# Kernel optimization log

Hardware: AMD Instinct MI355X
Metric: run time of the kernel (lower is better)

The kernel has to match this reference:

```python
import jax, jax.numpy as jnp
import numpy as np

B, N, K, CLS = 256, 15, 520, 800  # batch, points per streamline, k+k_global, classes
EPS = 1e-5


def _bn(x, g, b, m, v, axis=1):
    # eval-mode BatchNorm with running stats
    shape = [1] * x.ndim
    shape[axis] = -1
    rs = lambda a: a.reshape(shape)
    return rs(g) * (x - rs(m)) * jax.lax.rsqrt(rs(v) + EPS) + rs(b)


def setup_inputs():
    key = jax.random.key(0)
    kit = iter(jax.random.split(key, 24))
    nk = lambda: next(kit)
    p = {}
    p["pts"] = jax.random.normal(nk(), (B, N, 3), jnp.float32)
    p["label"] = jax.random.randint(nk(), (B,), 0, CLS)
    p["info_point_set"] = jax.random.normal(nk(), (B, K, N, 3), jnp.float32)

    def lin(cout, cin):
        w = jax.random.normal(nk(), (cout, cin), jnp.float32) * (1.0 / np.sqrt(cin))
        return w, jnp.zeros((cout,), jnp.float32)

    def bn(c):
        return (jnp.ones((c,), jnp.float32), jnp.zeros((c,), jnp.float32),
                jax.random.normal(nk(), (c,), jnp.float32) * 0.05,
                jnp.ones((c,), jnp.float32))

    p["w_info"], p["b_info"] = lin(64, 6)
    p["g_info"], p["be_info"], p["m_info"], p["v_info"] = bn(64)
    p["w2"], p["b2"] = lin(128, 64)
    p["g2"], p["be2"], p["m2"], p["v2"] = bn(128)
    p["w3"], p["b3"] = lin(1024, 128)
    p["g3"], p["be3"], p["m3"], p["v3"] = bn(1024)
    p["wf1"], p["bf1"] = lin(512, 1024)
    p["gf1"], p["bef1"], p["mf1"], p["vf1"] = bn(512)
    p["wf2"], p["bf2"] = lin(256, 512)
    p["gf2"], p["bef2"], p["mf2"], p["vf2"] = bn(256)
    p["wf3"], p["bf3"] = lin(CLS, 256)
    return p


def reference(pts, label, info_point_set,
              w_info, b_info, g_info, be_info, m_info, v_info,
              w2, b2, g2, be2, m2, v2,
              w3, b3, g3, be3, m3, v3,
              wf1, bf1, gf1, bef1, mf1, vf1,
              wf2, bf2, gf2, bef2, mf2, vf2,
              wf3, bf3):
    x = jnp.transpose(pts, (0, 2, 1))                      # [B,3,N]
    ips = jnp.transpose(info_point_set, (0, 3, 2, 1))      # [B,3,N,K]
    xr = jnp.broadcast_to(x[..., None], ips.shape)         # [B,3,N,K]
    h = jnp.concatenate([ips - xr, xr], axis=1)            # [B,6,N,K]
    h = jnp.einsum('oc,bcnk->bonk', w_info, h) + b_info[None, :, None, None]
    h = jax.nn.relu(_bn(h, g_info, be_info, m_info, v_info))
    h = jnp.max(h, axis=-1)                                # [B,64,N]  (max over neighbors)
    h2 = jax.nn.relu(_bn(jnp.einsum('oc,bcn->bon', w2, h) + b2[None, :, None],
                         g2, be2, m2, v2))                 # [B,128,N]
    h3 = _bn(jnp.einsum('oc,bcn->bon', w3, h2) + b3[None, :, None],
             g3, be3, m3, v3)                              # [B,1024,N]
    g = jnp.max(h3, axis=2)                                # [B,1024] global max-pool
    f1 = jax.nn.relu(_bn(g @ wf1.T + bf1, gf1, bef1, mf1, vf1, axis=1))
    f2 = jax.nn.relu(_bn(f1 @ wf2.T + bf2, gf2, bef2, mf2, vf2, axis=1))  # dropout identity (eval)
    ret = f2 @ wf3.T + bf3                                 # [B,CLS]
    return (ret, f2)
```

## Files before the change

### kernel.cpp

```cpp
#include <hip/hip_runtime.h>
#include <math.h>

#define EPS 1e-5f

typedef __attribute__((ext_vector_type(8))) short short8v;
typedef __attribute__((ext_vector_type(4))) float f32x4;
typedef __attribute__((ext_vector_type(16))) float f32x16;

__device__ __forceinline__ unsigned short bf16r(float x) {
    unsigned u = __float_as_uint(x);
    return (unsigned short)((u + 0x7FFFu + ((u >> 16) & 1u)) >> 16);
}
__device__ __forceinline__ float bf2f(unsigned short h) {
    return __uint_as_float(((unsigned)h) << 16);
}
__device__ __forceinline__ unsigned packhl(float x) {
    const unsigned short h = bf16r(x);
    const unsigned short l = bf16r(x - bf2f(h));
    return (unsigned)h | ((unsigned)l << 16);
}

__global__ __launch_bounds__(256) void k_pre(
    const float* __restrict__ w3, const float* __restrict__ b3,
    const float* __restrict__ g3, const float* __restrict__ be3,
    const float* __restrict__ m3, const float* __restrict__ v3,
    const float* __restrict__ w2, const float* __restrict__ b2,
    const float* __restrict__ g2, const float* __restrict__ be2,
    const float* __restrict__ m2, const float* __restrict__ v2,
    const float* __restrict__ w_info, const float* __restrict__ b_info,
    const float* __restrict__ g_info, const float* __restrict__ be_info,
    const float* __restrict__ m_info, const float* __restrict__ v_info,
    const float* __restrict__ bf1, const float* __restrict__ gf1,
    const float* __restrict__ bef1, const float* __restrict__ mf1,
    const float* __restrict__ vf1,
    const float* __restrict__ bf2, const float* __restrict__ gf2,
    const float* __restrict__ bef2, const float* __restrict__ mf2,
    const float* __restrict__ vf2,
    const float* __restrict__ wf1, const float* __restrict__ wf2,
    const float* __restrict__ wf3,
    unsigned short* __restrict__ Bh, unsigned short* __restrict__ Bl,
    float* __restrict__ bias3,
    float4* __restrict__ w2q, float* __restrict__ bias2,
    unsigned short* __restrict__ Bedge,
    float4* __restrict__ qTab4,
    float* __restrict__ sf1, float* __restrict__ cf1,
    float* __restrict__ sf2, float* __restrict__ cf2,
    unsigned short* __restrict__ B1h, unsigned short* __restrict__ B1l,
    unsigned short* __restrict__ B2h, unsigned short* __restrict__ B2l,
    unsigned short* __restrict__ B3h, unsigned short* __restrict__ B3l)
{
    const int blk = blockIdx.x, tid = threadIdx.x;
    if (blk < 64) {
        const int t = blk * 256 + tid;
        const int kt = t >> 12;
        const int nt = (t >> 6) & 63;
        const int lane = t & 63;
        const int o  = nt * 16 + (lane & 15);
        const int kb = kt * 32 + ((lane >> 4) << 3);
        const float a3 = g3[o] * rsqrtf(v3[o] + EPS);
        #pragma unroll
        for (int j = 0; j < 8; ++j) {
            const float wv = a3 * w3[(size_t)o * 128 + kb + j];
            const unsigned short hi = bf16r(wv);
            Bh[(size_t)t * 8 + j] = hi;
            Bl[(size_t)t * 8 + j] = bf16r(wv - bf2f(hi));
        }
    } else if (blk == 64) {
        for (int idx = tid; idx < 2048; idx += 256) {
            const int o2 = idx & 127, cq = idx >> 7;
            const float a2 = g2[o2] * rsqrtf(v2[o2] + EPS);
            const float4 w = *(const float4*)(w2 + (size_t)o2 * 64 + cq * 4);
            w2q[cq * 128 + o2] = make_float4(a2 * w.x, a2 * w.y, a2 * w.z, a2 * w.w);
        }
        if (tid < 128) {
            const float a2 = g2[tid] * rsqrtf(v2[tid] + EPS);
            bias2[tid] = a2 * (b2[tid] - m2[tid]) + be2[tid];
        }
    } else if (blk == 65) {
        if (tid < 128) {
            const int nt = tid >> 6, lane = tid & 63;
            const int grp = lane >> 5;
            const int o = nt * 32 + (lane & 31);
            const float a = g_info[o] * rsqrtf(v_info[o] + EPS);
            const float c0 = a * w_info[o*6+0];
            const float c1 = a * w_info[o*6+1];
            const float c2 = a * w_info[o*6+2];
            const unsigned short ch0 = bf16r(c0), ch1 = bf16r(c1), ch2 = bf16r(c2);
            const unsigned short cl0 = bf16r(c0 - bf2f(ch0));
            const unsigned short cl1 = bf16r(c1 - bf2f(ch1));
            const unsigned short cl2 = bf16r(c2 - bf2f(ch2));
            unsigned short out[8] = {0,0,0,0,0,0,0,0};
            if (grp == 0) {
                out[0]=ch0; out[1]=ch1; out[2]=ch2;
                out[3]=cl0; out[4]=cl1; out[5]=cl2;
                out[6]=ch0; out[7]=ch1;
            } else {
                out[0]=ch2;
            }
            #pragma unroll
            for (int j = 0; j < 8; ++j)
                Bedge[(size_t)(nt*64 + lane)*8 + j] = out[j];
        }
        if (tid < 64) {
            const int o = tid;
            const float w0 = w_info[o*6+0], w1 = w_info[o*6+1], w2c = w_info[o*6+2];
            const float w3c = w_info[o*6+3], w4 = w_info[o*6+4], w5 = w_info[o*6+5];
            const float a = g_info[o] * rsqrtf(v_info[o] + EPS);
            qTab4[o] = make_float4(a*(w3c-w0), a*(w4-w1), a*(w5-w2c),
                                   a*(b_info[o]-m_info[o]) + be_info[o]);
        }
        for (int c = tid; c < 1024; c += 256) {
            const float a3 = g3[c] * rsqrtf(v3[c] + EPS);
            bias3[c] = a3 * (b3[c] - m3[c]) + be3[c];
        }
        for (int c = tid; c < 512; c += 256) {
            const float s = gf1[c] * rsqrtf(vf1[c] + EPS);
            sf1[c] = s;
            cf1[c] = s * (bf1[c] - mf1[c]) + bef1[c];
        }
        {
            const int c = tid;
            const float s = gf2[c] * rsqrtf(vf2[c] + EPS);
            sf2[c] = s;
            cf2[c] = s * (bf2[c] - mf2[c]) + bef2[c];
        }
    } else if (blk < 322) {
        const int idx = (blk - 66) * 256 + tid;
        const int lane = idx & 63;
        const int nt = (idx >> 6) & 15;
        const int kt = idx >> 10;
        const int n  = nt * 32 + (lane & 31);
        const int kb = kt * 16 + ((lane >> 5) << 3);
        #pragma unroll
        for (int j = 0; j < 8; ++j) {
            const float wv = wf1[(size_t)n * 1024 + kb + j];
            const unsigned short hi = bf16r(wv);
            B1h[(size_t)idx * 8 + j] = hi;
            B1l[(size_t)idx * 8 + j] = bf16r(wv - bf2f(hi));
        }
    } else if (blk < 386) {
        const int idx = (blk - 322) * 256 + tid;
        const int lane = idx & 63;
        const int nt = (idx >> 6) & 7;
        const int kt = idx >> 9;
        const int n  = nt * 32 + (lane & 31);
        const int kb = kt * 16 + ((lane >> 5) << 3);
        #pragma unroll
        for (int j = 0; j < 8; ++j) {
            const float wv = wf2[(size_t)n * 512 + kb + j];
            const unsigned short hi = bf16r(wv);
            B2h[(size_t)idx * 8 + j] = hi;
            B2l[(size_t)idx * 8 + j] = bf16r(wv - bf2f(hi));
        }
    } else {
        const int idx = (blk - 386) * 256 + tid;
        const int lane = idx & 63;
        const int g6 = idx >> 6;
        const int nt = g6 % 25;
        const int kt = g6 / 25;
        const int n  = nt * 32 + (lane & 31);
        const int kb = kt * 16 + ((lane >> 5) << 3);
        #pragma unroll
        for (int j = 0; j < 8; ++j) {
            const float wv = wf3[(size_t)n * 256 + kb + j];
            const unsigned short hi = bf16r(wv);
            B3h[(size_t)idx * 8 + j] = hi;
            B3l[(size_t)idx * 8 + j] = bf16r(wv - bf2f(hi));
        }
    }
}

__global__ __launch_bounds__(960) void k_edgeS3(
    const float* __restrict__ pts,
    const float* __restrict__ info,
    const unsigned short* __restrict__ Bedge,
    const float4* __restrict__ qTab4,
    const float4* __restrict__ w2q,
    const float* __restrict__ bias2,
    const unsigned short* __restrict__ Bh,
    const unsigned short* __restrict__ Bl,
    const float* __restrict__ bias3,
    unsigned short* __restrict__ ghi,
    unsigned short* __restrict__ glo)
{
    __shared__ unsigned dsb[23400];
    __shared__ float h1s[960];
    __shared__ unsigned short h2hL[2048];
    __shared__ unsigned short h2lL[2048];

    const int tid = threadIdx.x;
    const int b = blockIdx.x;

    {
        const float4* src = (const float4*)(info + (size_t)b * 23400);
        uint4* dst = (uint4*)dsb;
        for (int i = tid; i < 5850; i += 960) {
            const float4 v = src[i];
            uint4 pv;
            pv.x = packhl(v.x); pv.y = packhl(v.y);
            pv.z = packhl(v.z); pv.w = packhl(v.w);
            dst[i] = pv;
        }
    }
    __syncthreads();

    const int wave = tid >> 6, lane = tid & 63;
    const int la = lane & 31;
    const bool hiHalf = lane >= 32;

    {
        short8v bfrag0 = *(const short8v*)(Bedge + (size_t)(0*64 + lane)*8);
        short8v bfrag1 = *(const short8v*)(Bedge + (size_t)(1*64 + lane)*8);

        const f32x16 zero16 = {0.f,0.f,0.f,0.f,0.f,0.f,0.f,0.f,
                               0.f,0.f,0.f,0.f,0.f,0.f,0.f,0.f};

        {
            const int n = wave;
            float m0 = -INFINITY, m1 = -INFINITY;
            const unsigned* pb = dsb + n*3;

            unsigned w0 = 0, w1 = 0, w2 = 0;
            {
                const unsigned* p = pb + la*45;
                if (!hiHalf) { w0 = p[0]; w1 = p[1]; }
                w2 = p[2];
            }

            #pragma unroll 1
            for (int mt = 0; mt < 17; ++mt) {
                unsigned nw0 = 0, nw1 = 0, nw2 = 0;
                if (mt < 16) {
                    int nrow = (mt+1)*32 + la;
                    nrow = nrow > 519 ? 519 : nrow;
                    const unsigned* p = pb + nrow*45;
                    if (!hiHalf) { nw0 = p[0]; nw1 = p[1]; }
                    nw2 = p[2];
                }
                int4 ai;
                if (!hiHalf) {
                    ai.x = (int)((w0 & 0xFFFFu) | (w1 << 16));
                    ai.y = (int)((w2 & 0xFFFFu) | (w0 << 16));
                    ai.z = (int)((w1 & 0xFFFFu) | (w2 << 16));
                    ai.w = (int)((w0 >> 16) | (w1 & 0xFFFF0000u));
                } else {
                    ai.x = (int)(w2 >> 16);
                    ai.y = 0; ai.z = 0; ai.w = 0;
                }
                const short8v afrag = *(short8v*)&ai;
                const f32x16 r0 = __builtin_amdgcn_mfma_f32_32x32x16_bf16(afrag, bfrag0, zero16, 0,0,0);
                const f32x16 r1 = __builtin_amdgcn_mfma_f32_32x32x16_bf16(afrag, bfrag1, zero16, 0,0,0);
                #pragma unroll
                for (int c = 0; c < 16; c += 4) {
                    m0 = fmaxf(m0, fmaxf(fmaxf(r0[c], r0[c+1]),
                                         fmaxf(r0[c+2], r0[c+3])));
                    m1 = fmaxf(m1, fmaxf(fmaxf(r1[c], r1[c+1]),
                                         fmaxf(r1[c+2], r1[c+3])));
                }
                w0 = nw0; w1 = nw1; w2 = nw2;
            }
            m0 = fmaxf(m0, __shfl_xor(m0, 32));
            m1 = fmaxf(m1, __shfl_xor(m1, 32));

            if (lane < 32) {
                const float x0 = pts[b*45 + n*3 + 0];
                const float x1 = pts[b*45 + n*3 + 1];
                const float x2 = pts[b*45 + n*3 + 2];
                {
                    const int o = lane;
                    const float4 qv = qTab4[o];
                    const float bias = fmaf(qv.x, x0, fmaf(qv.y, x1, fmaf(qv.z, x2, qv.w)));
                    h1s[n*64 + o] = fmaxf(m0 + bias, 0.f);
                }
                {
                    const int o = 32 + lane;
                    const float4 qv = qTab4[o];
                    const float bias = fmaf(qv.x, x0, fmaf(qv.y, x1, fmaf(qv.z, x2, qv.w)));
                    h1s[n*64 + o] = fmaxf(m1 + bias, 0.f);
                }
            }
        }
    }
    __syncthreads();

    for (int idx = tid; idx < 2048; idx += 960) {
        const int o2 = idx & 127, n = idx >> 7;
        float val = 0.f;
        if (n < 15) {
            float acc = 0.f;
            #pragma unroll
            for (int cq = 0; cq < 16; ++cq) {
                const float4 h4 = *(const float4*)(&h1s[n*64 + cq*4]);
                const float4 w4 = w2q[cq*128 + o2];
                acc = fmaf(w4.x, h4.x, fmaf(w4.y, h4.y,
                      fmaf(w4.z, h4.z, fmaf(w4.w, h4.w, acc))));
            }
            val = fmaxf(acc + bias2[o2], 0.f);
        }
        const unsigned short hi = bf16r(val);
        const unsigned short lo = bf16r(val - bf2f(hi));
        h2hL[idx] = hi;
        h2lL[idx] = lo;
    }
    __syncthreads();

    {
        const int arow = lane & 15, agrp = lane >> 4;

        short8v ahi[4], alo[4];
        {
            const unsigned short* Ab = h2hL + arow*128 + agrp*8;
            const unsigned short* Al = h2lL + arow*128 + agrp*8;
            #pragma unroll
            for (int kt = 0; kt < 4; ++kt) {
                ahi[kt] = *(const short8v*)(Ab + kt*32);
                alo[kt] = *(const short8v*)(Al + kt*32);
            }
        }

        for (int nt = wave; nt < 64; nt += 15) {
            f32x4 a0 = {0.f, 0.f, 0.f, 0.f};
            f32x4 a1 = a0, a2 = a0;
            #pragma unroll
            for (int kt = 0; kt < 4; ++kt) {
                const size_t off = (((size_t)kt*64 + nt)*64 + lane) * 8;
                const short8v bh = *(const short8v*)(Bh + off);
                const short8v bl = *(const short8v*)(Bl + off);
                a0 = __builtin_amdgcn_mfma_f32_16x16x32_bf16(ahi[kt], bh, a0, 0, 0, 0);
                a1 = __builtin_amdgcn_mfma_f32_16x16x32_bf16(ahi[kt], bl, a1, 0, 0, 0);
                a2 = __builtin_amdgcn_mfma_f32_16x16x32_bf16(alo[kt], bh, a2, 0, 0, 0);
            }
            const float r0 = a0[0] + a1[0] + a2[0];
            const float r1 = a0[1] + a1[1] + a2[1];
            const float r2 = a0[2] + a1[2] + a2[2];
            const float r3 = a0[3] + a1[3] + a2[3];
            float m = fmaxf(fmaxf(r0, r1), r2);
            if (agrp != 3) m = fmaxf(m, r3);
            m = fmaxf(m, __shfl_xor(m, 16));
            m = fmaxf(m, __shfl_xor(m, 32));
            if (lane < 16) {
                const float val = m + bias3[nt*16 + lane];
                const unsigned short hi = bf16r(val);
                ghi[(size_t)b*1024 + nt*16 + lane] = hi;
                glo[(size_t)b*1024 + nt*16 + lane] = bf16r(val - bf2f(hi));
            }
        }
    }
}

__global__ __launch_bounds__(256) void k_fc1m(
    const unsigned short* __restrict__ gh,
    const unsigned short* __restrict__ gl,
    const unsigned short* __restrict__ B1h,
    const unsigned short* __restrict__ B1l,
    const float* __restrict__ sf1, const float* __restrict__ cf1,
    unsigned short* __restrict__ f1h,
    unsigned short* __restrict__ f1l)
{
    __shared__ float part[4][32][33];

    const int tid = threadIdx.x;
    const int bm = blockIdx.x * 32, bn = blockIdx.y * 32;
    const int wave = tid >> 6, lane = tid & 63;
    const int m = bm + (lane & 31);
    const int kgrp = (lane >> 5) << 3;

    f32x16 acc = {0.f,0.f,0.f,0.f,0.f,0.f,0.f,0.f,
                  0.f,0.f,0.f,0.f,0.f,0.f,0.f,0.f};

    for (int kt = wave*16; kt < wave*16 + 16; ++kt) {
        const int kb = kt*16 + kgrp;
        const short8v ah = *(const short8v*)(gh + (size_t)m*1024 + kb);
        const short8v al = *(const short8v*)(gl + (size_t)m*1024 + kb);
        const size_t boff = ((size_t)kt*1024 + blockIdx.y*64 + lane) * 8;
        const short8v bh = *(const short8v*)(B1h + boff);
        const short8v bl = *(const short8v*)(B1l + boff);
        acc = __builtin_amdgcn_mfma_f32_32x32x16_bf16(ah, bh, acc, 0,0,0);
        acc = __builtin_amdgcn_mfma_f32_32x32x16_bf16(ah, bl, acc, 0,0,0);
        acc = __builtin_amdgcn_mfma_f32_32x32x16_bf16(al, bh, acc, 0,0,0);
    }
    {
        const int n = lane & 31, mhl = (lane >> 5) << 2;
        #pragma unroll
        for (int reg = 0; reg < 16; ++reg) {
            const int mrow = (reg & 3) + 8*(reg >> 2) + mhl;
            part[wave][mrow][n] = acc[reg];
        }
    }
    __syncthreads();

    for (int i = tid; i < 1024; i += 256) {
        const int lm = i >> 5, ln = i & 31;
        const float sum = part[0][lm][ln] + part[1][lm][ln]
                        + part[2][lm][ln] + part[3][lm][ln];
        const int ch = bn + ln;
        const float val = fmaxf(fmaf(sf1[ch], sum, cf1[ch]), 0.f);
        const unsigned short hi = bf16r(val);
        f1h[(size_t)(bm + lm)*512 + ch] = hi;
        f1l[(size_t)(bm + lm)*512 + ch] = bf16r(val - bf2f(hi));
    }
}

__global__ __launch_bounds__(256) void k_fc2m(
    const unsigned short* __restrict__ f1h,
    const unsigned short* __restrict__ f1l,
    const unsigned short* __restrict__ B2h,
    const unsigned short* __restrict__ B2l,
    const float* __restrict__ sf2, const float* __restrict__ cf2,
    float* __restrict__ f2out,
    unsigned short* __restrict__ f2h,
    unsigned short* __restrict__ f2l)
{
    __shared__ float part[4][32][33];

    const int tid = threadIdx.x;
    const int bm = blockIdx.x * 32, bn = blockIdx.y * 32;
    const int wave = tid >> 6, lane = tid & 63;
    const int m = bm + (lane & 31);
    const int kgrp = (lane >> 5) << 3;

    f32x16 acc = {0.f,0.f,0.f,0.f,0.f,0.f,0.f,0.f,
                  0.f,0.f,0.f,0.f,0.f,0.f,0.f,0.f};

    for (int kt = wave*8; kt < wave*8 + 8; ++kt) {
        const int kb = kt*16 + kgrp;
        const short8v ah = *(const short8v*)(f1h + (size_t)m*512 + kb);
        const short8v al = *(const short8v*)(f1l + (size_t)m*512 + kb);
        const size_t boff = ((size_t)kt*512 + blockIdx.y*64 + lane) * 8;
        const short8v bh = *(const short8v*)(B2h + boff);
        const short8v bl = *(const short8v*)(B2l + boff);
        acc = __builtin_amdgcn_mfma_f32_32x32x16_bf16(ah, bh, acc, 0,0,0);
        acc = __builtin_amdgcn_mfma_f32_32x32x16_bf16(ah, bl, acc, 0,0,0);
        acc = __builtin_amdgcn_mfma_f32_32x32x16_bf16(al, bh, acc, 0,0,0);
    }
    {
        const int n = lane & 31, mhl = (lane >> 5) << 2;
        #pragma unroll
        for (int reg = 0; reg < 16; ++reg) {
            const int mrow = (reg & 3) + 8*(reg >> 2) + mhl;
            part[wave][mrow][n] = acc[reg];
        }
    }
    __syncthreads();

    for (int i = tid; i < 1024; i += 256) {
        const int lm = i >> 5, ln = i & 31;
        const float sum = part[0][lm][ln] + part[1][lm][ln]
                        + part[2][lm][ln] + part[3][lm][ln];
        const int ch = bn + ln;
        const float val = fmaxf(fmaf(sf2[ch], sum, cf2[ch]), 0.f);
        const size_t o = (size_t)(bm + lm)*256 + ch;
        f2out[o] = val;
        const unsigned short hi = bf16r(val);
        f2h[o] = hi;
        f2l[o] = bf16r(val - bf2f(hi));
    }
}

__global__ __launch_bounds__(256) void k_fc3m(
    const unsigned short* __restrict__ f2h,
    const unsigned short* __restrict__ f2l,
    const unsigned short* __restrict__ B3h,
    const unsigned short* __restrict__ B3l,
    const float* __restrict__ bias,
    float* __restrict__ C)
{
    __shared__ float part[4][32][33];

    const int tid = threadIdx.x;
    const int bm = blockIdx.x * 32;
    const int wave = tid >> 6, lane = tid & 63;
    const int m = bm + (lane & 31);
    const int kgrp = (lane >> 5) << 3;

    f32x16 acc = {0.f,0.f,0.f,0.f,0.f,0.f,0.f,0.f,
                  0.f,0.f,0.f,0.f,0.f,0.f,0.f,0.f};

    for (int kt = wave*4; kt < wave*4 + 4; ++kt) {
        const int kb = kt*16 + kgrp;
        const short8v ah = *(const short8v*)(f2h + (size_t)m*256 + kb);
        const short8v al = *(const short8v*)(f2l + (size_t)m*256 + kb);
        const size_t boff = (((size_t)kt*25 + blockIdx.y)*64 + lane) * 8;
        const short8v bh = *(const short8v*)(B3h + boff);
        const short8v bl = *(const short8v*)(B3l + boff);
        acc = __builtin_amdgcn_mfma_f32_32x32x16_bf16(ah, bh, acc, 0,0,0);
        acc = __builtin_amdgcn_mfma_f32_32x32x16_bf16(ah, bl, acc, 0,0,0);
        acc = __builtin_amdgcn_mfma_f32_32x32x16_bf16(al, bh, acc, 0,0,0);
    }
    {
        const int n = lane & 31, mhl = (lane >> 5) << 2;
        #pragma unroll
        for (int reg = 0; reg < 16; ++reg) {
            const int mrow = (reg & 3) + 8*(reg >> 2) + mhl;
            part[wave][mrow][n] = acc[reg];
        }
    }
    __syncthreads();

    for (int i = tid; i < 1024; i += 256) {
        const int lm = i >> 5, ln = i & 31;
        const float sum = part[0][lm][ln] + part[1][lm][ln]
                        + part[2][lm][ln] + part[3][lm][ln];
        const int ch = blockIdx.y * 32 + ln;
        C[(size_t)(bm + lm)*800 + ch] = sum + bias[ch];
    }
}

extern "C" void kernel_launch(void* const* d_in, const int* in_sizes, int n_in,
                              void* d_out, int out_size, void* d_ws, size_t ws_size,
                              hipStream_t stream)
{
    const float* pts     = (const float*)d_in[0];
    const float* info    = (const float*)d_in[2];
    const float* w_info  = (const float*)d_in[3];
    const float* b_info  = (const float*)d_in[4];
    const float* g_info  = (const float*)d_in[5];
    const float* be_info = (const float*)d_in[6];
    const float* m_info  = (const float*)d_in[7];
    const float* v_info  = (const float*)d_in[8];
    const float* w2      = (const float*)d_in[9];
    const float* b2      = (const float*)d_in[10];
    const float* g2      = (const float*)d_in[11];
    const float* be2     = (const float*)d_in[12];
    const float* m2      = (const float*)d_in[13];
    const float* v2      = (const float*)d_in[14];
    const float* w3      = (const float*)d_in[15];
    const float* b3      = (const float*)d_in[16];
    const float* g3      = (const float*)d_in[17];
    const float* be3     = (const float*)d_in[18];
    const float* m3      = (const float*)d_in[19];
    const float* v3      = (const float*)d_in[20];
    const float* wf1     = (const float*)d_in[21];
    const float* bf1     = (const float*)d_in[22];
    const float* gf1     = (const float*)d_in[23];
    const float* bef1    = (const float*)d_in[24];
    const float* mf1     = (const float*)d_in[25];
    const float* vf1     = (const float*)d_in[26];
    const float* wf2     = (const float*)d_in[27];
    const float* bf2     = (const float*)d_in[28];
    const float* gf2     = (const float*)d_in[29];
    const float* bef2    = (const float*)d_in[30];
    const float* mf2     = (const float*)d_in[31];
    const float* vf2     = (const float*)d_in[32];
    const float* wf3     = (const float*)d_in[33];
    const float* bf3     = (const float*)d_in[34];

    float* ws = (float*)d_ws;
    unsigned short* ghi   = (unsigned short*)(ws + 0);
    unsigned short* glo   = (unsigned short*)(ws + 131072);
    unsigned short* f2h   = (unsigned short*)(ws + 0);
    unsigned short* f2l   = (unsigned short*)(ws + 32768);
    unsigned short* f1h   = (unsigned short*)(ws + 262144);
    unsigned short* f1l   = (unsigned short*)(ws + 327680);
    unsigned short* B1h   = (unsigned short*)(ws + 393216);
    unsigned short* B1l   = (unsigned short*)(ws + 655360);
    unsigned short* B2h   = (unsigned short*)(ws + 917504);
    unsigned short* B2l   = (unsigned short*)(ws + 983040);
    unsigned short* B3h   = (unsigned short*)(ws + 1048576);
    unsigned short* B3l   = (unsigned short*)(ws + 1150976);
    unsigned short* Bh    = (unsigned short*)(ws + 1277952);
    unsigned short* Bl    = (unsigned short*)(ws + 1343488);
    float*          bias3 = ws + 1409024;
    float4*         w2q   = (float4*)(ws + 1410048);
    float*          bias2 = ws + 1418240;
    float4*         qTab4 = (float4*)(ws + 1418624);
    float*          sf1   = ws + 1418880;
    float*          cf1   = ws + 1419392;
    float*          sf2   = ws + 1419904;
    float*          cf2   = ws + 1420160;
    unsigned short* Bedge = (unsigned short*)(ws + 1420416);

    float* ret = (float*)d_out;
    float* f2  = ret + 256 * 800;

    k_pre<<<486, 256, 0, stream>>>(
        w3, b3, g3, be3, m3, v3,
        w2, b2, g2, be2, m2, v2,
        w_info, b_info, g_info, be_info, m_info, v_info,
        bf1, gf1, bef1, mf1, vf1,
        bf2, gf2, bef2, mf2, vf2,
        wf1, wf2, wf3,
        Bh, Bl, bias3, w2q, bias2, Bedge, qTab4, sf1, cf1, sf2, cf2,
        B1h, B1l, B2h, B2l, B3h, B3l);

    k_edgeS3<<<256, 960, 0, stream>>>(pts, info, Bedge, qTab4,
                                      w2q, bias2, Bh, Bl, bias3, ghi, glo);

    k_fc1m<<<dim3(8, 16), 256, 0, stream>>>(ghi, glo, B1h, B1l,
                                            sf1, cf1, f1h, f1l);

    k_fc2m<<<dim3(8, 8), 256, 0, stream>>>(f1h, f1l, B2h, B2l,
                                           sf2, cf2, f2, f2h, f2l);

    k_fc3m<<<dim3(8, 25), 256, 0, stream>>>(f2h, f2l, B3h, B3l, bf3, ret);
}
```

Before: 55.84 us.

## Fuse three FC GEMM kernels into one cooperative kernel with grid syncs

Replaces the three separate fc1/fc2/fc3 kernel launches with a single cooperative kernel of 200 blocks. The stages are separated by grid-wide barriers, and blocks beyond each stage's tile count sit idle until the barrier. The aim is to remove two kernel launch gaps and the dependency bubbles between them. In exchange it pays for the grid.sync barriers and relies on the cooperative launch being supported and all 200 blocks being co-resident.

```diff
diff --git a/kernel.cpp b/kernel.cpp
--- a/kernel.cpp
+++ b/kernel.cpp
@@ -1,4 +1,5 @@
 #include <hip/hip_runtime.h>
+#include <hip/hip_cooperative_groups.h>
 #include <math.h>
 
 #define EPS 1e-5f
@@ -348,161 +349,141 @@
     }
 }
 
-__global__ __launch_bounds__(256) void k_fc1m(
+__global__ __launch_bounds__(256) void k_fcAll(
     const unsigned short* __restrict__ gh,
     const unsigned short* __restrict__ gl,
-    const unsigned short* __restrict__ B1h,
-    const unsigned short* __restrict__ B1l,
+    const unsigned short* __restrict__ B1h, const unsigned short* __restrict__ B1l,
     const float* __restrict__ sf1, const float* __restrict__ cf1,
-    unsigned short* __restrict__ f1h,
-    unsigned short* __restrict__ f1l)
-{
-    __shared__ float part[4][32][33];
-
-    const int tid = threadIdx.x;
-    const int bm = blockIdx.x * 32, bn = blockIdx.y * 32;
-    const int wave = tid >> 6, lane = tid & 63;
-    const int m = bm + (lane & 31);
-    const int kgrp = (lane >> 5) << 3;
-
-    f32x16 acc = {0.f,0.f,0.f,0.f,0.f,0.f,0.f,0.f,
-                  0.f,0.f,0.f,0.f,0.f,0.f,0.f,0.f};
-
-    for (int kt = wave*16; kt < wave*16 + 16; ++kt) {
-        const int kb = kt*16 + kgrp;
-        const short8v ah = *(const short8v*)(gh + (size_t)m*1024 + kb);
-        const short8v al = *(const short8v*)(gl + (size_t)m*1024 + kb);
-        const size_t boff = ((size_t)kt*1024 + blockIdx.y*64 + lane) * 8;
-        const short8v bh = *(const short8v*)(B1h + boff);
-        const short8v bl = *(const short8v*)(B1l + boff);
-        acc = __builtin_amdgcn_mfma_f32_32x32x16_bf16(ah, bh, acc, 0,0,0);
-        acc = __builtin_amdgcn_mfma_f32_32x32x16_bf16(ah, bl, acc, 0,0,0);
-        acc = __builtin_amdgcn_mfma_f32_32x32x16_bf16(al, bh, acc, 0,0,0);
-    }
-    {
-        const int n = lane & 31, mhl = (lane >> 5) << 2;
-        #pragma unroll
-        for (int reg = 0; reg < 16; ++reg) {
-            const int mrow = (reg & 3) + 8*(reg >> 2) + mhl;
-            part[wave][mrow][n] = acc[reg];
-        }
-    }
-    __syncthreads();
-
-    for (int i = tid; i < 1024; i += 256) {
-        const int lm = i >> 5, ln = i & 31;
-        const float sum = part[0][lm][ln] + part[1][lm][ln]
-                        + part[2][lm][ln] + part[3][lm][ln];
-        const int ch = bn + ln;
-        const float val = fmaxf(fmaf(sf1[ch], sum, cf1[ch]), 0.f);
-        const unsigned short hi = bf16r(val);
-        f1h[(size_t)(bm + lm)*512 + ch] = hi;
-        f1l[(size_t)(bm + lm)*512 + ch] = bf16r(val - bf2f(hi));
-    }
-}
-
-__global__ __launch_bounds__(256) void k_fc2m(
-    const unsigned short* __restrict__ f1h,
-    const unsigned short* __restrict__ f1l,
-    const unsigned short* __restrict__ B2h,
-    const unsigned short* __restrict__ B2l,
+    unsigned short* __restrict__ f1h, unsigned short* __restrict__ f1l,
+    const unsigned short* __restrict__ B2h, const unsigned short* __restrict__ B2l,
     const float* __restrict__ sf2, const float* __restrict__ cf2,
     float* __restrict__ f2out,
-    unsigned short* __restrict__ f2h,
-    unsigned short* __restrict__ f2l)
-{
-    __shared__ float part[4][32][33];
-
-    const int tid = threadIdx.x;
-    const int bm = blockIdx.x * 32, bn = blockIdx.y * 32;
-    const int wave = tid >> 6, lane = tid & 63;
-    const int m = bm + (lane & 31);
-    const int kgrp = (lane >> 5) << 3;
-
-    f32x16 acc = {0.f,0.f,0.f,0.f,0.f,0.f,0.f,0.f,
-                  0.f,0.f,0.f,0.f,0.f,0.f,0.f,0.f};
-
-    for (int kt = wave*8; kt < wave*8 + 8; ++kt) {
-        const int kb = kt*16 + kgrp;
-        const short8v ah = *(const short8v*)(f1h + (size_t)m*512 + kb);
-        const short8v al = *(const short8v*)(f1l + (size_t)m*512 + kb);
-        const size_t boff = ((size_t)kt*512 + blockIdx.y*64 + lane) * 8;
-        const short8v bh = *(const short8v*)(B2h + boff);
-        const short8v bl = *(const short8v*)(B2l + boff);
-        acc = __builtin_amdgcn_mfma_f32_32x32x16_bf16(ah, bh, acc, 0,0,0);
-        acc = __builtin_amdgcn_mfma_f32_32x32x16_bf16(ah, bl, acc, 0,0,0);
-        acc = __builtin_amdgcn_mfma_f32_32x32x16_bf16(al, bh, acc, 0,0,0);
-    }
-    {
-        const int n = lane & 31, mhl = (lane >> 5) << 2;
-        #pragma unroll
-        for (int reg = 0; reg < 16; ++reg) {
-            const int mrow = (reg & 3) + 8*(reg >> 2) + mhl;
-            part[wave][mrow][n] = acc[reg];
-        }
-    }
-    __syncthreads();
-
-    for (int i = tid; i < 1024; i += 256) {
-        const int lm = i >> 5, ln = i & 31;
-        const float sum = part[0][lm][ln] + part[1][lm][ln]
-                        + part[2][lm][ln] + part[3][lm][ln];
-        const int ch = bn + ln;
-        const float val = fmaxf(fmaf(sf2[ch], sum, cf2[ch]), 0.f);
-        const size_t o = (size_t)(bm + lm)*256 + ch;
-        f2out[o] = val;
-        const unsigned short hi = bf16r(val);
-        f2h[o] = hi;
-        f2l[o] = bf16r(val - bf2f(hi));
-    }
-}
-
-__global__ __launch_bounds__(256) void k_fc3m(
-    const unsigned short* __restrict__ f2h,
-    const unsigned short* __restrict__ f2l,
-    const unsigned short* __restrict__ B3h,
-    const unsigned short* __restrict__ B3l,
-    const float* __restrict__ bias,
+    unsigned short* __restrict__ f2h, unsigned short* __restrict__ f2l,
+    const unsigned short* __restrict__ B3h, const unsigned short* __restrict__ B3l,
+    const float* __restrict__ bias3fc,
     float* __restrict__ C)
 {
+    namespace cg = cooperative_groups;
+    cg::grid_group gridg = cg::this_grid();
+
     __shared__ float part[4][32][33];
 
+    const int blk = blockIdx.x;
     const int tid = threadIdx.x;
-    const int bm = blockIdx.x * 32;
     const int wave = tid >> 6, lane = tid & 63;
-    const int m = bm + (lane & 31);
     const int kgrp = (lane >> 5) << 3;
-
-    f32x16 acc = {0.f,0.f,0.f,0.f,0.f,0.f,0.f,0.f,
-                  0.f,0.f,0.f,0.f,0.f,0.f,0.f,0.f};
-
-    for (int kt = wave*4; kt < wave*4 + 4; ++kt) {
-        const int kb = kt*16 + kgrp;
-        const short8v ah = *(const short8v*)(f2h + (size_t)m*256 + kb);
-        const short8v al = *(const short8v*)(f2l + (size_t)m*256 + kb);
-        const size_t boff = (((size_t)kt*25 + blockIdx.y)*64 + lane) * 8;
-        const short8v bh = *(const short8v*)(B3h + boff);
-        const short8v bl = *(const short8v*)(B3l + boff);
-        acc = __builtin_amdgcn_mfma_f32_32x32x16_bf16(ah, bh, acc, 0,0,0);
-        acc = __builtin_amdgcn_mfma_f32_32x32x16_bf16(ah, bl, acc, 0,0,0);
-        acc = __builtin_amdgcn_mfma_f32_32x32x16_bf16(al, bh, acc, 0,0,0);
-    }
+    const f32x16 z16 = {0.f,0.f,0.f,0.f,0.f,0.f,0.f,0.f,
+                        0.f,0.f,0.f,0.f,0.f,0.f,0.f,0.f};
+
+    if (blk < 128) {
+        const int bm = (blk & 7) * 32, bny = blk >> 3;
+        const int m = bm + (lane & 31);
+        f32x16 acc = z16;
+        for (int kt = wave*16; kt < wave*16 + 16; ++kt) {
+            const int kb = kt*16 + kgrp;
+            const short8v ah = *(const short8v*)(gh + (size_t)m*1024 + kb);
+            const short8v al = *(const short8v*)(gl + (size_t)m*1024 + kb);
+            const size_t boff = ((size_t)kt*1024 + bny*64 + lane) * 8;
+            const short8v bh = *(const short8v*)(B1h + boff);
+            const short8v bl = *(const short8v*)(B1l + boff);
+            acc = __builtin_amdgcn_mfma_f32_32x32x16_bf16(ah, bh, acc, 0,0,0);
+            acc = __builtin_amdgcn_mfma_f32_32x32x16_bf16(ah, bl, acc, 0,0,0);
+            acc = __builtin_amdgcn_mfma_f32_32x32x16_bf16(al, bh, acc, 0,0,0);
+        }
+        {
+            const int n = lane & 31, mhl = (lane >> 5) << 2;
+            #pragma unroll
+            for (int reg = 0; reg < 16; ++reg) {
+                const int mrow = (reg & 3) + 8*(reg >> 2) + mhl;
+                part[wave][mrow][n] = acc[reg];
+            }
+        }
+        __syncthreads();
+        for (int i = tid; i < 1024; i += 256) {
+            const int lm = i >> 5, ln = i & 31;
+            const float sum = part[0][lm][ln] + part[1][lm][ln]
+                            + part[2][lm][ln] + part[3][lm][ln];
+            const int ch = bny*32 + ln;
+            const float val = fmaxf(fmaf(sf1[ch], sum, cf1[ch]), 0.f);
+            const unsigned short hi = bf16r(val);
+            f1h[(size_t)(bm + lm)*512 + ch] = hi;
+            f1l[(size_t)(bm + lm)*512 + ch] = bf16r(val - bf2f(hi));
+        }
+    }
+    gridg.sync();
+
+    if (blk < 64) {
+        const int bm = (blk & 7) * 32, bny = blk >> 3;
+        const int m = bm + (lane & 31);
+        f32x16 acc = z16;
+        for (int kt = wave*8; kt < wave*8 + 8; ++kt) {
+            const int kb = kt*16 + kgrp;
+            const short8v ah = *(const short8v*)(f1h + (size_t)m*512 + kb);
+            const short8v al = *(const short8v*)(f1l + (size_t)m*512 + kb);
+            const size_t boff = ((size_t)kt*512 + bny*64 + lane) * 8;
+            const short8v bh = *(const short8v*)(B2h + boff);
+            const short8v bl = *(const short8v*)(B2l + boff);
+            acc = __builtin_amdgcn_mfma_f32_32x32x16_bf16(ah, bh, acc, 0,0,0);
+            acc = __builtin_amdgcn_mfma_f32_32x32x16_bf16(ah, bl, acc, 0,0,0);
+            acc = __builtin_amdgcn_mfma_f32_32x32x16_bf16(al, bh, acc, 0,0,0);
+        }
+        {
+            const int n = lane & 31, mhl = (lane >> 5) << 2;
+            #pragma unroll
+            for (int reg = 0; reg < 16; ++reg) {
+                const int mrow = (reg & 3) + 8*(reg >> 2) + mhl;
+                part[wave][mrow][n] = acc[reg];
+            }
+        }
+        __syncthreads();
+        for (int i = tid; i < 1024; i += 256) {
+            const int lm = i >> 5, ln = i & 31;
+            const float sum = part[0][lm][ln] + part[1][lm][ln]
+                            + part[2][lm][ln] + part[3][lm][ln];
+            const int ch = bny*32 + ln;
+            const float val = fmaxf(fmaf(sf2[ch], sum, cf2[ch]), 0.f);
+            const size_t o = (size_t)(bm + lm)*256 + ch;
+            f2out[o] = val;
+            const unsigned short hi = bf16r(val);
+            f2h[o] = hi;
+            f2l[o] = bf16r(val - bf2f(hi));
+        }
+    }
+    gridg.sync();
+
     {
-        const int n = lane & 31, mhl = (lane >> 5) << 2;
-        #pragma unroll
-        for (int reg = 0; reg < 16; ++reg) {
-            const int mrow = (reg & 3) + 8*(reg >> 2) + mhl;
-            part[wave][mrow][n] = acc[reg];
-        }
-    }
-    __syncthreads();
-
-    for (int i = tid; i < 1024; i += 256) {
-        const int lm = i >> 5, ln = i & 31;
-        const float sum = part[0][lm][ln] + part[1][lm][ln]
-                        + part[2][lm][ln] + part[3][lm][ln];
-        const int ch = blockIdx.y * 32 + ln;
-        C[(size_t)(bm + lm)*800 + ch] = sum + bias[ch];
+        const int bm = (blk & 7) * 32;
+        const int nty = blk >> 3;
+        const int m = bm + (lane & 31);
+        f32x16 acc = z16;
+        for (int kt = wave*4; kt < wave*4 + 4; ++kt) {
+            const int kb = kt*16 + kgrp;
+            const short8v ah = *(const short8v*)(f2h + (size_t)m*256 + kb);
+            const short8v al = *(const short8v*)(f2l + (size_t)m*256 + kb);
+            const size_t boff = (((size_t)kt*25 + nty)*64 + lane) * 8;
+            const short8v bh = *(const short8v*)(B3h + boff);
+            const short8v bl = *(const short8v*)(B3l + boff);
+            acc = __builtin_amdgcn_mfma_f32_32x32x16_bf16(ah, bh, acc, 0,0,0);
+            acc = __builtin_amdgcn_mfma_f32_32x32x16_bf16(ah, bl, acc, 0,0,0);
+            acc = __builtin_amdgcn_mfma_f32_32x32x16_bf16(al, bh, acc, 0,0,0);
+        }
+        __syncthreads();
+        {
+            const int n = lane & 31, mhl = (lane >> 5) << 2;
+            #pragma unroll
+            for (int reg = 0; reg < 16; ++reg) {
+                const int mrow = (reg & 3) + 8*(reg >> 2) + mhl;
+                part[wave][mrow][n] = acc[reg];
+            }
+        }
+        __syncthreads();
+        for (int i = tid; i < 1024; i += 256) {
+            const int lm = i >> 5, ln = i & 31;
+            const float sum = part[0][lm][ln] + part[1][lm][ln]
+                            + part[2][lm][ln] + part[3][lm][ln];
+            const int ch = nty * 32 + ln;
+            C[(size_t)(bm + lm)*800 + ch] = sum + bias3fc[ch];
+        }
     }
 }
 
@@ -586,11 +567,16 @@
     k_edgeS3<<<256, 960, 0, stream>>>(pts, info, Bedge, qTab4,
                                       w2q, bias2, Bh, Bl, bias3, ghi, glo);
 
-    k_fc1m<<<dim3(8, 16), 256, 0, stream>>>(ghi, glo, B1h, B1l,
-                                            sf1, cf1, f1h, f1l);
-
-    k_fc2m<<<dim3(8, 8), 256, 0, stream>>>(f1h, f1l, B2h, B2l,
-                                           sf2, cf2, f2, f2h, f2l);
-
-    k_fc3m<<<dim3(8, 25), 256, 0, stream>>>(f2h, f2l, B3h, B3l, bf3, ret);
-}
+    {
+        void* args[] = {
+            (void*)&ghi, (void*)&glo,
+            (void*)&B1h, (void*)&B1l, (void*)&sf1, (void*)&cf1,
+            (void*)&f1h, (void*)&f1l,
+            (void*)&B2h, (void*)&B2l, (void*)&sf2, (void*)&cf2,
+            (void*)&f2, (void*)&f2h, (void*)&f2l,
+            (void*)&B3h, (void*)&B3l, (void*)&bf3, (void*)&ret
+        };
+        hipLaunchCooperativeKernel((void*)k_fcAll, dim3(200), dim3(256),
+                                   args, 0, stream);
+    }
+}
```

Result: slower. 110.9 us (+98.6%).
